# Performance work log

Measured on AMD Instinct MI355X. Metric: run time of the kernel, lower is better.

The kernel has to match this reference:

```python
import jax, jax.numpy as jnp
import numpy as np

CODEBOOK_SIZE = 8192
CODEBOOK_DIM = 16
IN_DIM = 512


def setup_inputs() -> dict:
    key = jax.random.key(0)
    k1, k2, k3 = jax.random.split(key, 3)
    input_values = jax.random.normal(k1, (8, 4096, IN_DIM), dtype=jnp.float32)
    # xavier_uniform for Linear(IN_DIM -> CODEBOOK_DIM), weight shape (out, in) in torch
    limit = float(np.sqrt(6.0 / (IN_DIM + CODEBOOK_DIM)))
    proj_weight = jax.random.uniform(k2, (CODEBOOK_DIM, IN_DIM), dtype=jnp.float32, minval=-limit, maxval=limit)
    code_book = jax.random.normal(k3, (CODEBOOK_SIZE, CODEBOOK_DIM), dtype=jnp.float32)
    return {"input_values": input_values, "proj_weight": proj_weight, "code_book": code_book}


def reference(input_values, proj_weight, code_book):
    # targets: (B, L, d) = input @ W^T  (bias-free random projection)
    targets = jnp.einsum("bld,cd->blc", input_values, proj_weight)  # (B, L, 16)
    # Squared L2 distance via expansion ||t - c||^2 = ||t||^2 - 2 t.c + ||c||^2.
    # argmin is identical to argmin of the norm; avoids the (B,L,K,d) broadcast tensor.
    t_sq = jnp.sum(targets * targets, axis=-1, keepdims=True)        # (B, L, 1)
    c_sq = jnp.sum(code_book * code_book, axis=-1)                   # (K,)
    cross = jnp.einsum("blc,kc->blk", targets, code_book)            # (B, L, K)
    dist_sq = t_sq - 2.0 * cross + c_sq                              # (B, L, K)
    labels = jnp.argmin(dist_sq, axis=-1)                            # (B, L) int
    return labels
```

## Files before the change

### kernel.cpp

```cpp
#include <hip/hip_runtime.h>
#include <stdint.h>

#define IN_DIM 512
#define CB 8192
#define CD 16
#define NROWS 32768
#define DELTAQ 1.5e-2f
#define FMAXV 3.402823466e38f

typedef short bf16x8 __attribute__((ext_vector_type(8)));
typedef float f32x4 __attribute__((ext_vector_type(4)));

__device__ inline unsigned short f2bf(float x) {
    unsigned u = __float_as_uint(x);
    unsigned r = u + 0x7FFFu + ((u >> 16) & 1u);
    return (unsigned short)(r >> 16);
}
__device__ inline float bf2f(unsigned short h) { return __uint_as_float(((unsigned)h) << 16); }
__device__ inline unsigned umin32(unsigned a, unsigned b) { return a < b ? a : b; }
__device__ inline unsigned umax32(unsigned a, unsigned b) { return a > b ? a : b; }
__device__ inline unsigned long long shfl_xor_u64(unsigned long long x, int m) {
    double d = __shfl_xor(__longlong_as_double((long long)x), m, 64);
    return (unsigned long long)__double_as_longlong(d);
}

__global__ __launch_bounds__(256) void prep_kernel(const float* __restrict__ cb,
                                                   float* __restrict__ csq,
                                                   float* __restrict__ csqoff,
                                                   bf16x8* __restrict__ Bp) {
    int id = blockIdx.x * 256 + threadIdx.x;
    if (id < CB) {
        const float4* p = (const float4*)(cb + (size_t)id * CD);
        float s = 0.f;
#pragma unroll
        for (int j = 0; j < 4; ++j) {
            float4 v = p[j];
            s += v.x * v.x + v.y * v.y + v.z * v.z + v.w * v.w;
        }
        csq[id] = s;
        csqoff[id] = s + 256.0f;
    }
    int slot = id & 63;
    int nt = id >> 6;
    int q = slot >> 4;
    int n = nt * 16 + (slot & 15);
    int d0 = (q & 1) * 8;
    bool lo = (q < 2);
    const float* src = cb + (size_t)n * CD + d0;
    bf16x8 v;
#pragma unroll
    for (int j = 0; j < 8; ++j) {
        float x = src[j];
        unsigned short a = f2bf(x);
        unsigned short b = f2bf(x - bf2f(a));
        v[j] = (short)(lo ? a : b);
    }
    Bp[id] = v;
}

__global__ __launch_bounds__(256) void proj_partial_kernel(const float* __restrict__ in,
                                                           const float* __restrict__ W,
                                                           float* __restrict__ partials) {
    __shared__ float4 LIN[2048];
    int tid = threadIdx.x;
    int lane = tid & 63;
    int dg = __builtin_amdgcn_readfirstlane(tid >> 6);
    int strip = blockIdx.x >> 2;
    int c = blockIdx.x & 3;
    int rowbase = strip * 64;
    const float4* inp4 = (const float4*)in;

#pragma unroll
    for (int u = 0; u < 8; ++u) {
        int f = tid + u * 256;
        int r = f >> 5, o = f & 31;
        LIN[r * 32 + (o ^ (r & 7))] = inp4[(size_t)(rowbase + r) * 128 + c * 32 + o];
    }
    __syncthreads();

    float acc[4];
#pragma unroll
    for (int i = 0; i < 4; ++i) acc[i] = 0.f;
#pragma unroll 4
    for (int j = 0; j < 32; ++j) {
        float4 v = LIN[lane * 32 + (j ^ (lane & 7))];
#pragma unroll
        for (int i = 0; i < 4; ++i) {
            const float* w = W + (size_t)(4 * dg + i) * IN_DIM + c * 128 + j * 4;
            acc[i] += v.x * w[0] + v.y * w[1] + v.z * w[2] + v.w * w[3];
        }
    }
    float* o = partials + (size_t)c * NROWS * CD + (size_t)(rowbase + lane) * CD + 4 * dg;
#pragma unroll
    for (int i = 0; i < 4; ++i) o[i] = acc[i];
}

__global__ __launch_bounds__(256) void proj_combine_kernel(const float* __restrict__ partials,
                                                           float* __restrict__ tprime) {
    int idx = blockIdx.x * 256 + threadIdx.x;
    const size_t P = (size_t)NROWS * CD;
    float p0 = partials[idx];
    float p1 = partials[P + idx];
    float p2 = partials[2 * P + idx];
    float p3 = partials[3 * P + idx];
    tprime[idx] = -2.f * (((p0 + p1) + p2) + p3);
}

__global__ __launch_bounds__(512, 8) void scan_kernel(
        const float* __restrict__ tprime, const float* __restrict__ csq,
        const float* __restrict__ csqoff, const bf16x8* __restrict__ Bp,
        const float* __restrict__ cb, int* __restrict__ out) {
    __shared__ float tbuf[32][17];
    __shared__ unsigned long long m_k[32][8];
    __shared__ unsigned m_s2[32][8];
    __shared__ int flagged[32];
    __shared__ unsigned long long red[8];

    int tid = threadIdx.x;
    int lane = tid & 63;
    int e = __builtin_amdgcn_readfirstlane(tid >> 6);
    int rowbase = blockIdx.x * 32;

    if (tid < 512) {
        tbuf[tid >> 4][tid & 15] = tprime[(size_t)rowbase * CD + tid];
    }
    __syncthreads();

    int q = lane >> 4;
    int col = lane & 15;
    int d0 = (q & 1) * 8;
    bool lo = (q < 2);

    bf16x8 A1[2], A2[2];
#pragma unroll
    for (int g = 0; g < 2; ++g) {
        int arow = 16 * g + col;
#pragma unroll
        for (int j = 0; j < 8; ++j) {
            float x = tbuf[arow][d0 + j];
            unsigned short t1 = f2bf(x);
            unsigned short t2 = f2bf(x - bf2f(t1));
            A1[g][j] = (short)t1;
            A2[g][j] = (short)(lo ? t2 : 0);
        }
    }

    unsigned s1[2][4], s2[2][4];
#pragma unroll
    for (int g = 0; g < 2; ++g)
#pragma unroll
        for (int r = 0; r < 4; ++r) { s1[g][r] = 0xFFFFFFFFu; s2[g][r] = 0xFFFFFFFFu; }

    int nt0 = e * 64;
    const bf16x8* pb = Bp + (size_t)nt0 * 64 + lane;
    const float* csqp = csqoff + nt0 * 16 + col;

#pragma unroll 4
    for (int t = 0; t < 64; ++t) {
        bf16x8 b = pb[(size_t)t * 64];
        float cs = csqp[t * 16];
        f32x4 ini = {cs, cs, cs, cs};
        unsigned tt = (unsigned)t;
#pragma unroll
        for (int g = 0; g < 2; ++g) {
            f32x4 acc = __builtin_amdgcn_mfma_f32_16x16x32_bf16(A1[g], b, ini, 0, 0, 0);
            acc = __builtin_amdgcn_mfma_f32_16x16x32_bf16(A2[g], b, acc, 0, 0, 0);
#pragma unroll
            for (int r = 0; r < 4; ++r) {
                unsigned k = (__float_as_uint(acc[r]) & 0xFFFFFFC0u) | tt;
                s2[g][r] = umin32(s2[g][r], umax32(k, s1[g][r]));
                s1[g][r] = umin32(s1[g][r], k);
            }
        }
    }

#pragma unroll
    for (int g = 0; g < 2; ++g)
#pragma unroll
        for (int r = 0; r < 4; ++r) {
            unsigned long long FK = ((unsigned long long)(s1[g][r] & 0xFFFFFFC0u) << 13)
                                  | ((unsigned long long)e << 10)
                                  | ((unsigned long long)(s1[g][r] & 63u) << 4)
                                  | (unsigned long long)col;
            unsigned s2q = s2[g][r] & 0xFFFFFFC0u;
#pragma unroll
            for (int m = 1; m < 16; m <<= 1) {
                unsigned long long oFK = shfl_xor_u64(FK, m);
                unsigned os2 = (unsigned)__shfl_xor((int)s2q, m, 64);
                unsigned qa = (unsigned)(FK >> 13);
                unsigned qb = (unsigned)(oFK >> 13);
                s2q = umin32(umin32(s2q, os2), umax32(qa, qb));
                FK = oFK < FK ? oFK : FK;
            }
            if (col == 0) {
                int rl = 16 * g + 4 * q + r;
                m_k[rl][e] = FK;
                m_s2[rl][e] = s2q;
            }
        }
    __syncthreads();

    if (tid < 32) {
        unsigned long long mFK = m_k[tid][0];
        unsigned g1 = (unsigned)(m_k[tid][0] >> 13);
        unsigned g2 = m_s2[tid][0];
#pragma unroll
        for (int ee = 1; ee < 8; ++ee) {
            unsigned long long F = m_k[tid][ee];
            unsigned u = (unsigned)(F >> 13);
            if (u < g1) { g2 = g1; g1 = u; } else { g2 = umin32(g2, u); }
            g2 = umin32(g2, m_s2[tid][ee]);
            mFK = F < mFK ? F : mFK;
        }
        int ccol = (int)(mFK & 15ull);
        int ctile = (int)((mFK >> 4) & 63ull);
        int ce = (int)((mFK >> 10) & 7ull);
        out[rowbase + tid] = ((ce * 64 + ctile) << 4) | ccol;
        flagged[tid] = (__uint_as_float(g2) - __uint_as_float(g1) < DELTAQ) ? 1 : 0;
    }
    __syncthreads();

    for (int fi = 0; fi < 32; ++fi) {
        if (!flagged[fi]) continue;
        int row = rowbase + fi;
        float tp[16];
#pragma unroll
        for (int d = 0; d < 16; ++d) tp[d] = tbuf[fi][d];
        float best = FMAXV;
        int bidx = 0;
#pragma unroll 2
        for (int ii = 0; ii < 16; ++ii) {
            int k = tid + 512 * ii;
            const float* cp = cb + (size_t)k * CD;
            float s = csq[k];
#pragma unroll
            for (int d = 0; d < 16; ++d) s += tp[d] * cp[d];
            if (s < best) { best = s; bidx = k; }
        }
        unsigned u = __float_as_uint(best);
        u = (u & 0x80000000u) ? ~u : (u | 0x80000000u);
        unsigned long long key = ((unsigned long long)u << 32) | (unsigned)bidx;
#pragma unroll
        for (int m = 1; m < 64; m <<= 1) {
            unsigned long long o = shfl_xor_u64(key, m);
            key = o < key ? o : key;
        }
        if (lane == 0) red[e] = key;
        __syncthreads();
        if (tid == 0) {
            unsigned long long mm = red[0];
#pragma unroll
            for (int i = 1; i < 8; ++i) { unsigned long long x = red[i]; mm = x < mm ? x : mm; }
            out[row] = (int)(mm & 0xFFFFFFFFull);
        }
        __syncthreads();
    }
}

extern "C" void kernel_launch(void* const* d_in, const int* in_sizes, int n_in,
                              void* d_out, int out_size, void* d_ws, size_t ws_size,
                              hipStream_t stream) {
    const float* input = (const float*)d_in[0];
    const float* W     = (const float*)d_in[1];
    const float* cb    = (const float*)d_in[2];
    int* out = (int*)d_out;

    float*  tprime   = (float*)d_ws;
    float*  csq      = tprime + (size_t)NROWS * CD;
    float*  csqoff   = csq + CB;
    bf16x8* Bp       = (bf16x8*)(csqoff + CB);
    float*  partials = (float*)(Bp + 32768);

    prep_kernel<<<32768 / 256, 256, 0, stream>>>(cb, csq, csqoff, Bp);
    proj_partial_kernel<<<(NROWS / 64) * 4, 256, 0, stream>>>(input, W, partials);
    proj_combine_kernel<<<NROWS * CD / 256, 256, 0, stream>>>(partials, tprime);
    scan_kernel<<<NROWS / 32, 512, 0, stream>>>(tprime, csq, csqoff, Bp, cb, out);
}
```

Before: 192.9 us.

## Move exact-rescan of ambiguous rows to a queued fallback kernel

The scan kernel no longer rescans close-call rows inline. Instead it appends them through an atomic counter to a global queue, and a separate fallback kernel redoes those rows in exact fp32 across 256 blocks. The ambiguity threshold is lowered, so fewer rows get flagged. The projection kernel now stages W in shared memory and transposes the input tile layout, and scan occupancy hints change from 8 to 6. The tighter threshold risks argmin mismatches where the split-bf16 MFMA error exceeds the new margin.

Measured after the change: 169.7 us. -12.0%, faster.

```diff
diff --git a/kernel.cpp b/kernel.cpp
--- a/kernel.cpp
+++ b/kernel.cpp
@@ -5,7 +5,7 @@
 #define CB 8192
 #define CD 16
 #define NROWS 32768
-#define DELTAQ 1.5e-2f
+#define DELTAQ 8e-3f
 #define FMAXV 3.402823466e38f
 
 typedef short bf16x8 __attribute__((ext_vector_type(8)));
@@ -27,8 +27,10 @@
 __global__ __launch_bounds__(256) void prep_kernel(const float* __restrict__ cb,
                                                    float* __restrict__ csq,
                                                    float* __restrict__ csqoff,
-                                                   bf16x8* __restrict__ Bp) {
+                                                   bf16x8* __restrict__ Bp,
+                                                   int* __restrict__ counter) {
     int id = blockIdx.x * 256 + threadIdx.x;
+    if (id == 0) counter[0] = 0;
     if (id < CB) {
         const float4* p = (const float4*)(cb + (size_t)id * CD);
         float s = 0.f;
@@ -62,6 +64,7 @@
                                                            const float* __restrict__ W,
                                                            float* __restrict__ partials) {
     __shared__ float4 LIN[2048];
+    __shared__ float4 WL[16 * 33];
     int tid = threadIdx.x;
     int lane = tid & 63;
     int dg = __builtin_amdgcn_readfirstlane(tid >> 6);
@@ -69,12 +72,19 @@
     int c = blockIdx.x & 3;
     int rowbase = strip * 64;
     const float4* inp4 = (const float4*)in;
-
+    const float4* W4 = (const float4*)W;
+
+#pragma unroll
+    for (int u = 0; u < 2; ++u) {
+        int f = tid + u * 256;
+        int d = f >> 5, o = f & 31;
+        WL[d * 33 + o] = W4[(size_t)d * 128 + c * 32 + o];
+    }
 #pragma unroll
     for (int u = 0; u < 8; ++u) {
         int f = tid + u * 256;
-        int r = f >> 5, o = f & 31;
-        LIN[r * 32 + (o ^ (r & 7))] = inp4[(size_t)(rowbase + r) * 128 + c * 32 + o];
+        int o = f & 31, r = f >> 5;
+        LIN[o * 64 + (r ^ (o & 7))] = inp4[(size_t)(rowbase + r) * 128 + c * 32 + o];
     }
     __syncthreads();
 
@@ -83,11 +93,11 @@
     for (int i = 0; i < 4; ++i) acc[i] = 0.f;
 #pragma unroll 4
     for (int j = 0; j < 32; ++j) {
-        float4 v = LIN[lane * 32 + (j ^ (lane & 7))];
+        float4 v = LIN[j * 64 + (lane ^ (j & 7))];
 #pragma unroll
         for (int i = 0; i < 4; ++i) {
-            const float* w = W + (size_t)(4 * dg + i) * IN_DIM + c * 128 + j * 4;
-            acc[i] += v.x * w[0] + v.y * w[1] + v.z * w[2] + v.w * w[3];
+            float4 w = WL[(4 * dg + i) * 33 + j];
+            acc[i] += v.x * w.x + v.y * w.y + v.z * w.z + v.w * w.w;
         }
     }
     float* o = partials + (size_t)c * NROWS * CD + (size_t)(rowbase + lane) * CD + 4 * dg;
@@ -106,24 +116,20 @@
     tprime[idx] = -2.f * (((p0 + p1) + p2) + p3);
 }
 
-__global__ __launch_bounds__(512, 8) void scan_kernel(
-        const float* __restrict__ tprime, const float* __restrict__ csq,
-        const float* __restrict__ csqoff, const bf16x8* __restrict__ Bp,
-        const float* __restrict__ cb, int* __restrict__ out) {
+__global__ __launch_bounds__(512, 6) void scan_kernel(
+        const float* __restrict__ tprime, const float* __restrict__ csqoff,
+        const bf16x8* __restrict__ Bp, int* __restrict__ out,
+        int* __restrict__ queue, int* __restrict__ counter) {
     __shared__ float tbuf[32][17];
     __shared__ unsigned long long m_k[32][8];
     __shared__ unsigned m_s2[32][8];
-    __shared__ int flagged[32];
-    __shared__ unsigned long long red[8];
 
     int tid = threadIdx.x;
     int lane = tid & 63;
     int e = __builtin_amdgcn_readfirstlane(tid >> 6);
     int rowbase = blockIdx.x * 32;
 
-    if (tid < 512) {
-        tbuf[tid >> 4][tid & 15] = tprime[(size_t)rowbase * CD + tid];
-    }
+    tbuf[tid >> 4][tid & 15] = tprime[(size_t)rowbase * CD + tid];
     __syncthreads();
 
     int q = lane >> 4;
@@ -215,22 +221,39 @@
         int ccol = (int)(mFK & 15ull);
         int ctile = (int)((mFK >> 4) & 63ull);
         int ce = (int)((mFK >> 10) & 7ull);
-        out[rowbase + tid] = ((ce * 64 + ctile) << 4) | ccol;
-        flagged[tid] = (__uint_as_float(g2) - __uint_as_float(g1) < DELTAQ) ? 1 : 0;
-    }
-    __syncthreads();
-
-    for (int fi = 0; fi < 32; ++fi) {
-        if (!flagged[fi]) continue;
-        int row = rowbase + fi;
+        int row = rowbase + tid;
+        out[row] = ((ce * 64 + ctile) << 4) | ccol;
+        if (__uint_as_float(g2) - __uint_as_float(g1) < DELTAQ) {
+            int pos = atomicAdd(counter, 1);
+            queue[pos] = row;
+        }
+    }
+}
+
+__global__ __launch_bounds__(256) void fallback_kernel(const float* __restrict__ tprime,
+                                                       const float* __restrict__ cb,
+                                                       const float* __restrict__ csq,
+                                                       const int* __restrict__ queue,
+                                                       const int* __restrict__ counter,
+                                                       int* __restrict__ out) {
+    __shared__ unsigned long long red[4];
+    int nq = counter[0];
+    int tid = threadIdx.x;
+    int lane = tid & 63;
+    int w = tid >> 6;
+
+    for (int qi = blockIdx.x; qi < nq; qi += 256) {
+        int row = queue[qi];
         float tp[16];
-#pragma unroll
-        for (int d = 0; d < 16; ++d) tp[d] = tbuf[fi][d];
+        const float* tpp = tprime + (size_t)row * CD;
+#pragma unroll
+        for (int d = 0; d < 16; ++d) tp[d] = tpp[d];
+
         float best = FMAXV;
         int bidx = 0;
 #pragma unroll 2
-        for (int ii = 0; ii < 16; ++ii) {
-            int k = tid + 512 * ii;
+        for (int i = 0; i < 32; ++i) {
+            int k = tid + 256 * i;
             const float* cp = cb + (size_t)k * CD;
             float s = csq[k];
 #pragma unroll
@@ -245,12 +268,12 @@
             unsigned long long o = shfl_xor_u64(key, m);
             key = o < key ? o : key;
         }
-        if (lane == 0) red[e] = key;
+        if (lane == 0) red[w] = key;
         __syncthreads();
         if (tid == 0) {
             unsigned long long mm = red[0];
 #pragma unroll
-            for (int i = 1; i < 8; ++i) { unsigned long long x = red[i]; mm = x < mm ? x : mm; }
+            for (int i = 1; i < 4; ++i) { unsigned long long x = red[i]; mm = x < mm ? x : mm; }
             out[row] = (int)(mm & 0xFFFFFFFFull);
         }
         __syncthreads();
@@ -270,9 +293,12 @@
     float*  csqoff   = csq + CB;
     bf16x8* Bp       = (bf16x8*)(csqoff + CB);
     float*  partials = (float*)(Bp + 32768);
-
-    prep_kernel<<<32768 / 256, 256, 0, stream>>>(cb, csq, csqoff, Bp);
+    int*    counter  = (int*)(partials + 4 * (size_t)NROWS * CD);
+    int*    queue    = counter + 16;
+
+    prep_kernel<<<32768 / 256, 256, 0, stream>>>(cb, csq, csqoff, Bp, counter);
     proj_partial_kernel<<<(NROWS / 64) * 4, 256, 0, stream>>>(input, W, partials);
     proj_combine_kernel<<<NROWS * CD / 256, 256, 0, stream>>>(partials, tprime);
-    scan_kernel<<<NROWS / 32, 512, 0, stream>>>(tprime, csq, csqoff, Bp, cb, out);
-}
+    scan_kernel<<<NROWS / 32, 512, 0, stream>>>(tprime, csqoff, Bp, out, queue, counter);
+    fallback_kernel<<<256, 256, 0, stream>>>(tprime, cb, csq, queue, counter, out);
+}
```
